# Kernel optimization log

Measured on AMD Instinct MI355X. Metric: run time of the kernel, lower is better.

Reference implementation:

```python
import jax, jax.numpy as jnp
import numpy as np

H = 64   # gru_hidden_dim == gnn_hidden_dim
F = 64   # node_feat_dim
K = 8    # k_nn
OUT = 32 # output_factor_dim
BN_EPS = 1e-5


def _gru_scan(x, Wih, Whh, bih, bhh):
    # x: [S, F] single sequence (torch bug makes GRU scan the b*n axis); returns [S, H]
    xp = x @ Wih.T + bih  # [S, 3H], gate order r,z,n (torch convention)
    def step(h, xt):
        hp = h @ Whh.T + bhh
        r = jax.nn.sigmoid(xt[:H] + hp[:H])
        z = jax.nn.sigmoid(xt[H:2 * H] + hp[H:2 * H])
        ng = jnp.tanh(xt[2 * H:] + r * hp[2 * H:])
        hn = (1.0 - z) * ng + z * h
        return hn, hn
    _, out = jax.lax.scan(step, jnp.zeros((H,), x.dtype), xp)
    return out


def _gcn_layer(x, row, col, w, W, b, n):
    # PyG GCNConv: out[col] += d^{-1/2}[row] * w * d^{-1/2}[col] * (x @ W.T)[row] + b
    xw = x @ W.T
    deg = jnp.zeros((n,), x.dtype).at[col].add(w)
    dinv = deg ** -0.5
    dinv = jnp.where(jnp.isinf(dinv), 0.0, dinv)
    norm = dinv[row] * w * dinv[col]
    out = jnp.zeros_like(xw).at[col].add(norm[:, None] * xw[row])
    return out + b


def setup_inputs() -> dict:
    key = jax.random.key(0)
    ks = jax.random.split(key, 20)
    s = 0.08  # ~ torch uniform(-1/sqrt(64), 1/sqrt(64)) scale
    d = {
        'x_seq': jax.random.normal(ks[0], (4, 8, F, 2048), jnp.float32),
        # gru_sim params
        'Wih_s': jax.random.normal(ks[1], (3 * H, F), jnp.float32) * s,
        'Whh_s': jax.random.normal(ks[2], (3 * H, H), jnp.float32) * s,
        'bih_s': jax.random.normal(ks[3], (3 * H,), jnp.float32) * s,
        'bhh_s': jax.random.normal(ks[4], (3 * H,), jnp.float32) * s,
        # gru params
        'Wih': jax.random.normal(ks[5], (3 * H, F), jnp.float32) * s,
        'Whh': jax.random.normal(ks[6], (3 * H, H), jnp.float32) * s,
        'bih': jax.random.normal(ks[7], (3 * H,), jnp.float32) * s,
        'bhh': jax.random.normal(ks[8], (3 * H,), jnp.float32) * s,
        # gcn1 / gcn2 params (GCNConv weight [out,in], bias [out])
        'W1': jax.random.normal(ks[9], (H, H), jnp.float32) * s,
        'b1': jnp.zeros((H,), jnp.float32),
        'W2': jax.random.normal(ks[10], (H, H), jnp.float32) * s,
        'b2': jnp.zeros((H,), jnp.float32),
        # batchnorm affine
        'gamma': jnp.ones((H,), jnp.float32),
        'beta': jnp.zeros((H,), jnp.float32),
        # predictor
        'Wp': jax.random.normal(ks[11], (OUT, H), jnp.float32) * s,
        'bp': jnp.zeros((OUT,), jnp.float32),
    }
    return d


def reference(x_seq, Wih_s, Whh_s, bih_s, bhh_s, Wih, Whh, bih, bhh,
              W1, b1, W2, b2, gamma, beta, Wp, bp):
    b, l, f, n = x_seq.shape
    # torch GRU is batch_first=True but fed [l, b*n, f]: it scans the b*n axis
    # as time and gru_out[-1] keeps only batch item l-1 -> only last time slice used.
    seq = x_seq[:, -1].transpose(0, 2, 1).reshape(b * n, f)  # [b*n, f]
    h = _gru_scan(seq, Wih_s, Whh_s, bih_s, bhh_s).reshape(b, n, H)      # gru_sim
    h_out = _gru_scan(seq, Wih, Whh, bih, bhh).reshape(b, n, H)          # gru

    # dynamic kNN graph from similarity
    sim = jnp.einsum('bni,bmi->bnm', h, h)
    eye = jnp.eye(n, dtype=bool)
    sim = jnp.where(eye[None], jnp.asarray(-1e9, sim.dtype), sim)
    vals, idx = jax.lax.top_k(sim, K)  # [b, n, K], sorted desc like torch.topk

    # edges: n*K knn edges + n unit-weight self loops (outer add_self_loops;
    # GCNConv's add_remaining_self_loops then adds nothing)
    row = jnp.concatenate([jnp.repeat(jnp.arange(n), K), jnp.arange(n)])

    def per_graph(v, ix, x):
        col = jnp.concatenate([ix.reshape(-1), jnp.arange(n)])
        w = jnp.concatenate([v.reshape(-1), jnp.ones((n,), v.dtype)])
        o1 = jax.nn.relu(_gcn_layer(x, row, col, w, W1, b1, n))
        o2 = jax.nn.relu(_gcn_layer(o1, row, col, w, W2, b2, n))
        return o2

    out2 = jax.vmap(per_graph)(vals, idx, h_out)  # [b, n, H]

    # BatchNorm1d (training mode: biased batch stats over b*n rows)
    flat = out2.reshape(b * n, H)
    mu = flat.mean(0)
    var = flat.var(0)
    normed = (flat - mu) / jnp.sqrt(var + BN_EPS) * gamma + beta

    out = normed @ Wp.T + bp
    return out.reshape(b, n, OUT)
```

## Files before the change

kernel.cpp:

```cpp
#include <hip/hip_runtime.h>
#include <hip/hip_bf16.h>

typedef __hip_bfloat16 bf16;

#define NB   4
#define NN   2048
#define NROW 8192
#define HD   64
#define G3   192
#define KNN  8
#define OUTD 32
#define SCHUNK 32
#define SBURN  96
#define NCH    256
#define SCH4   32
#define SBRN4  40
#define NCH4   256
#define TI   4
#define TOPB 256
#define XPR  32
#define SCR  32
#define TKR  16

#define OFF_FLAG  0u
#define OFF_DEG   64u
#define OFF_DINV  8256u
#define OFF_BNS   16448u
#define OFF_BNSQ  16512u
#define OFF_SCALE 16576u
#define OFF_SHIFT 16640u
#define OFF_VALS  16704u
#define OFF_IDX   82240u
#define OFF_A     147776u
#define OFF_C     672064u
#define OFF_XP0   1196352u
#define OFF_XP1   2769216u
#define OFF_END   4342080u

typedef __attribute__((ext_vector_type(8))) short short8v;
typedef __attribute__((ext_vector_type(4))) float f32x4;

__device__ __forceinline__ float sigmoidf_(float x) { return 1.f / (1.f + __expf(-x)); }
__device__ __forceinline__ float tanhf_(float x) {
    float e = __expf(-2.f * fabsf(x));
    float t = (1.f - e) / (1.f + e);
    return copysignf(t, x);
}
__device__ __forceinline__ float ld(const void* p, size_t i, int isbf) {
    return isbf ? __bfloat162float(((const bf16*)p)[i]) : ((const float*)p)[i];
}
__device__ __forceinline__ float bcast(float v, int k) {
    return __int_as_float(__builtin_amdgcn_readlane(__float_as_int(v), k));
}
__device__ __forceinline__ unsigned short bf16rne(float f) {
    unsigned u = __float_as_uint(f);
    return (unsigned short)((u + 0x7FFFu + ((u >> 16) & 1u)) >> 16);
}

__global__ void probe_kernel(const void* __restrict__ gamma, int* __restrict__ flag)
{
    unsigned w = ((const unsigned*)gamma)[0];
    *flag = (w == 0x3F800000u) ? 0 : 1;
}

__global__ __launch_bounds__(384) void xp_kernel(
    const void* __restrict__ x_seq,
    const void* __restrict__ Wih_s, const void* __restrict__ bih_s,
    const void* __restrict__ Wih,   const void* __restrict__ bih,
    float* __restrict__ xp0, float* __restrict__ xp1,
    const int* __restrict__ dtp)
{
    int isbf = *dtp;
    int row0 = blockIdx.x * XPR;
    int b = row0 >> 11, j0 = row0 & 2047;
    int t = threadIdx.x;

    __shared__ __align__(16) float S[XPR * 68];
    for (int idx = t; idx < XPR * HD; idx += 384) {
        int f = idx >> 5, jj = idx & (XPR - 1);
        S[jj * 68 + f] = ld(x_seq, (size_t)((b * 8 + 7) * 64 + f) * 2048 + (j0 + jj), isbf);
    }

    int g = t % G3;
    const void* W  = (t < G3) ? Wih_s : Wih;
    const void* bi = (t < G3) ? bih_s : bih;
    float* o = (t < G3) ? xp0 : xp1;
    float wreg[64];
    #pragma unroll
    for (int k = 0; k < 64; ++k) wreg[k] = ld(W, g * HD + k, isbf);
    float bias = ld(bi, g, isbf);
    __syncthreads();

    for (int jj = 0; jj < XPR; ++jj) {
        const float4* s4 = (const float4*)(S + jj * 68);
        float a0 = bias, a1 = 0.f, a2 = 0.f, a3 = 0.f;
        #pragma unroll
        for (int q = 0; q < 16; ++q) {
            float4 v = s4[q];
            a0 += wreg[4*q+0] * v.x;
            a1 += wreg[4*q+1] * v.y;
            a2 += wreg[4*q+2] * v.z;
            a3 += wreg[4*q+3] * v.w;
        }
        o[(size_t)(row0 + jj) * G3 + g] = (a0 + a1) + (a2 + a3);
    }
}

__global__ __launch_bounds__(128) void gru_scan_pack_kernel(
    const float* __restrict__ xp0, const float* __restrict__ xp1,
    const void* __restrict__ Whh_s, const void* __restrict__ bhh_s,
    const void* __restrict__ Whh,   const void* __restrict__ bhh,
    unsigned short* __restrict__ hAhi, unsigned short* __restrict__ hAlo,
    float* __restrict__ hC,
    const int* __restrict__ dtp)
{
    int isbf = *dtp;
    int gru = blockIdx.x >> 7;
    int pb  = blockIdx.x & 127;
    int w   = threadIdx.x >> 6;
    int L   = threadIdx.x & 63;
    int chunk = pb * 2 + w;
    const float* xpp = gru ? xp1 : xp0;
    const void* Wh   = gru ? Whh : Whh_s;
    const void* bh_p = gru ? bhh : bhh_s;

    __shared__ __align__(16) float4 SW4[64 * 64];

    for (int idx = threadIdx.x; idx < 64 * 64; idx += 128) {
        int k = idx >> 6, j = idx & 63;
        float4 v;
        v.x = ld(Wh, (size_t)j * 64 + k, isbf);
        v.y = ld(Wh, (size_t)(64 + j) * 64 + k, isbf);
        v.z = ld(Wh, (size_t)(128 + j) * 64 + k, isbf);
        v.w = 0.f;
        SW4[idx] = v;
    }
    float br  = ld(bh_p, L, isbf);
    float bz  = ld(bh_p, 64 + L, isbf);
    float bn_ = ld(bh_p, 128 + L, isbf);
    __syncthreads();

    int first = chunk * SCH4;
    int burn  = min(SBRN4, first);
    int start = first - burn;
    int steps = burn + SCH4;

    float hval = 0.f;
    size_t rb = (size_t)start * G3;
    float xr = xpp[rb + L];
    float xz = xpp[rb + 64 + L];
    float xn = xpp[rb + 128 + L];

    for (int t = 0; t < steps; ++t) {
        size_t nb = (size_t)min(start + t + 1, NROW - 1) * G3;
        float pxr = xpp[nb + L];
        float pxz = xpp[nb + 64 + L];
        float pxn = xpp[nb + 128 + L];

        float pr0 = br, pz0 = bz, pn0 = bn_;
        float pr1 = 0.f, pz1 = 0.f, pn1 = 0.f;
        #pragma unroll
        for (int k = 0; k < 64; k += 2) {
            float4 w0 = SW4[k * 64 + L];
            float4 w1 = SW4[(k + 1) * 64 + L];
            float b0 = bcast(hval, k);
            float b1 = bcast(hval, k + 1);
            pr0 += w0.x * b0; pz0 += w0.y * b0; pn0 += w0.z * b0;
            pr1 += w1.x * b1; pz1 += w1.y * b1; pn1 += w1.z * b1;
        }

        float r  = sigmoidf_(xr + pr0 + pr1);
        float z  = sigmoidf_(xz + pz0 + pz1);
        float ng = tanhf_(xn + r * (pn0 + pn1));
        hval = (1.f - z) * ng + z * hval;

        if (t >= burn) {
            size_t o = (size_t)(start + t) * HD + L;
            if (gru) {
                hC[o] = hval;
            } else {
                unsigned short hb = bf16rne(hval);
                float hf = __uint_as_float(((unsigned)hb) << 16);
                hAhi[o] = hb;
                hAlo[o] = bf16rne(hval - hf);
            }
        }
        xr = pxr; xz = pxz; xn = pxn;
    }
}

__global__ __launch_bounds__(192, 2) void gru_scan_fused_kernel(
    const void* __restrict__ x_seq,
    const void* __restrict__ Wih_s, const void* __restrict__ bih_s,
    const void* __restrict__ Whh_s, const void* __restrict__ bhh_s,
    const void* __restrict__ Wih,   const void* __restrict__ bih,
    const void* __restrict__ Whh,   const void* __restrict__ bhh,
    float* __restrict__ hA, float* __restrict__ hC,
    const int* __restrict__ dtp)
{
    int isbf = *dtp;
    int gru   = blockIdx.x >> 8;
    int chunk = blockIdx.x & 255;
    const void* Wh = gru ? Whh : Whh_s;
    const void* bh_p = gru ? bhh : bhh_s;
    const void* Wi = gru ? Wih : Wih_s;
    const void* bi_p = gru ? bih : bih_s;
    float* hout = gru ? hC : hA;

    int lane = threadIdx.x & 63;
    int w    = threadIdx.x >> 6;
    int g    = w * 64 + lane;

    float whh[64], wih[64];
    #pragma unroll
    for (int k = 0; k < 64; ++k) {
        whh[k] = ld(Wh, g * 64 + k, isbf);
        wih[k] = ld(Wi, g * 64 + k, isbf);
    }
    float bh = ld(bh_p, g, isbf);
    float bi = ld(bi_p, g, isbf);

    __shared__ float hs[64];
    __shared__ float ss[64];
    __shared__ float gr[64], gz[64], ga[64], gx[64];

    int first = chunk * SCHUNK;
    int burn  = min(SBURN, first);
    int start = first - burn;
    int steps = burn + SCHUNK;

    #define XIDX(r) ((size_t)((((r) >> 11) * 8 + 7) * 64 + lane) * 2048 + ((r) & 2047))
    float sf = 0.f;
    if (w == 0) {
        ss[lane] = ld(x_seq, XIDX(start), isbf);
        if (steps > 1) sf = ld(x_seq, XIDX(start + 1), isbf);
    }
    __syncthreads();

    float hval = 0.f;
    float sval = ss[lane];

    for (int t = 0; t < steps; ++t) {
        float a = bh, x = bi;
        #pragma unroll
        for (int k = 0; k < 64; ++k) {
            a += whh[k] * bcast(hval, k);
            x += wih[k] * bcast(sval, k);
        }
        if (w == 0)      gr[lane] = sigmoidf_(x + a);
        else if (w == 1) gz[lane] = sigmoidf_(x + a);
        else           { ga[lane] = a; gx[lane] = x; }
        __syncthreads();
        if (w == 0) {
            if (t + 1 < steps) {
                ss[lane] = sf;
                if (t + 2 < steps) sf = ld(x_seq, XIDX(start + t + 2), isbf);
            }
        } else if (w == 2) {
            float hn = (1.f - gz[lane]) * tanhf_(gx[lane] + gr[lane] * ga[lane])
                     + gz[lane] * hval;
            hs[lane] = hn;
            hval = hn;
            if (t >= burn) hout[(size_t)(start + t) * HD + lane] = hn;
        }
        __syncthreads();
        if (w != 2) hval = hs[lane];
        sval = ss[lane];
    }
    #undef XIDX
}

__device__ __forceinline__ void merge8(float tv[KNN], int tj[KNN], int off)
{
    float ov[KNN]; int oj[KNN];
    #pragma unroll
    for (int m = 0; m < KNN; ++m) {
        ov[m] = __shfl_xor(tv[m], off);
        oj[m] = __shfl_xor(tj[m], off);
    }
    #pragma unroll
    for (int m = 0; m < KNN; ++m) {
        if (ov[KNN - 1 - m] > tv[m]) { tv[m] = ov[KNN - 1 - m]; tj[m] = oj[KNN - 1 - m]; }
    }
    #pragma unroll
    for (int d = 4; d > 0; d >>= 1) {
        #pragma unroll
        for (int m = 0; m < KNN; ++m) {
            if ((m & d) == 0 && (m | d) < KNN) {
                int p = m | d;
                if (tv[p] > tv[m]) {
                    float fv = tv[m]; tv[m] = tv[p]; tv[p] = fv;
                    int fj = tj[m]; tj[m] = tj[p]; tj[p] = fj;
                }
            }
        }
    }
}

__global__ __launch_bounds__(512) void topk_mfma_kernel(
    const unsigned short* __restrict__ Ahi, const unsigned short* __restrict__ Alo,
    float* __restrict__ vals, int* __restrict__ idxs, float* __restrict__ deg)
{
    int bid = blockIdx.x;
    int row0 = bid * TKR;
    int bbase = row0 & ~(NN - 1);
    int rloc = row0 & (NN - 1);
    int t = threadIdx.x;
    int w = t >> 6, L = t & 63;
    int cL = L & 15, q = L >> 4;
    int chunk = q * 8;

    __shared__ float mv[8][TKR][KNN];
    __shared__ int   mj[8][TKR][KNN];

    size_t arow = (size_t)(row0 + cL) * HD;
    short8v ahi0 = *(const short8v*)(Ahi + arow + chunk);
    short8v ahi1 = *(const short8v*)(Ahi + arow + 32 + chunk);
    short8v alo0 = *(const short8v*)(Alo + arow + chunk);
    short8v alo1 = *(const short8v*)(Alo + arow + 32 + chunk);

    int jbase = w * 256;

    float tv[4][KNN]; int tj[4][KNN];
    #pragma unroll
    for (int e = 0; e < 4; ++e)
        #pragma unroll
        for (int m = 0; m < KNN; ++m) { tv[e][m] = -3e38f; tj[e][m] = 0; }

    #pragma unroll 1
    for (int strip = 0; strip < 4; ++strip) {
        #pragma unroll
        for (int g = 0; g < 4; ++g) {
            int j0 = jbase + strip * 64 + g * 16;
            size_t brow = (size_t)(bbase + j0 + cL) * HD;
            short8v bhi0 = *(const short8v*)(Ahi + brow + chunk);
            short8v bhi1 = *(const short8v*)(Ahi + brow + 32 + chunk);
            short8v blo0 = *(const short8v*)(Alo + brow + chunk);
            short8v blo1 = *(const short8v*)(Alo + brow + 32 + chunk);
            f32x4 accA = {0.f, 0.f, 0.f, 0.f};
            f32x4 accB = {0.f, 0.f, 0.f, 0.f};
            accA = __builtin_amdgcn_mfma_f32_16x16x32_bf16(ahi0, bhi0, accA, 0, 0, 0);
            accB = __builtin_amdgcn_mfma_f32_16x16x32_bf16(ahi0, blo0, accB, 0, 0, 0);
            accA = __builtin_amdgcn_mfma_f32_16x16x32_bf16(ahi1, bhi1, accA, 0, 0, 0);
            accB = __builtin_amdgcn_mfma_f32_16x16x32_bf16(ahi1, blo1, accB, 0, 0, 0);
            accA = __builtin_amdgcn_mfma_f32_16x16x32_bf16(alo0, bhi0, accA, 0, 0, 0);
            accB = __builtin_amdgcn_mfma_f32_16x16x32_bf16(alo1, bhi1, accB, 0, 0, 0);
            f32x4 acc = accA + accB;
            int jj = j0 + cL;
            #pragma unroll
            for (int e = 0; e < 4; ++e) {
                int r = q * 4 + e;
                float nv = (jj == rloc + r) ? -1e9f : acc[e];
                if (nv > tv[e][KNN - 1]) {
                    tv[e][KNN - 1] = nv; tj[e][KNN - 1] = jj;
                    #pragma unroll
                    for (int m = KNN - 1; m > 0; --m) {
                        if (tv[e][m] > tv[e][m - 1]) {
                            float fv = tv[e][m]; tv[e][m] = tv[e][m - 1]; tv[e][m - 1] = fv;
                            int fj = tj[e][m]; tj[e][m] = tj[e][m - 1]; tj[e][m - 1] = fj;
                        }
                    }
                }
            }
        }
    }

    #pragma unroll
    for (int e = 0; e < 4; ++e) {
        merge8(tv[e], tj[e], 1);
        merge8(tv[e], tj[e], 2);
        merge8(tv[e], tj[e], 4);
        merge8(tv[e], tj[e], 8);
    }
    if (cL == 0) {
        #pragma unroll
        for (int e = 0; e < 4; ++e)
            #pragma unroll
            for (int m = 0; m < KNN; ++m) {
                mv[w][q * 4 + e][m] = tv[e][m];
                mj[w][q * 4 + e][m] = tj[e][m];
            }
    }
    __syncthreads();

    if (w < 2) {
        int r = (w << 3) + (L >> 3);
        int p = L & 7;
        float fv[KNN]; int fj[KNN];
        #pragma unroll
        for (int m = 0; m < KNN; ++m) { fv[m] = mv[p][r][m]; fj[m] = mj[p][r][m]; }
        merge8(fv, fj, 1);
        merge8(fv, fj, 2);
        merge8(fv, fj, 4);
        if (p == 0) {
            int row = row0 + r;
            #pragma unroll
            for (int m = 0; m < KNN; ++m) {
                vals[(size_t)row * KNN + m] = fv[m];
                idxs[(size_t)row * KNN + m] = fj[m];
                atomicAdd(deg + bbase + fj[m], fv[m]);
            }
            atomicAdd(deg + row, 1.0f);
        }
    }
}

__global__ __launch_bounds__(TOPB, 2) void topk_kernel(
    const float* __restrict__ h,
    float* __restrict__ vals, int* __restrict__ idxs, float* __restrict__ deg)
{
    int bid = blockIdx.x;
    int b    = bid >> 9;
    int row0 = b * NN + (bid & 511) * TI;
    int i0 = row0 & 2047;
    int t = threadIdx.x;

    __shared__ __align__(16) float sim[TI][NN];
    __shared__ __align__(16) float hi[TI * HD];

    for (int q = t; q < TI * HD; q += TOPB)
        hi[q] = h[(size_t)(row0 + (q >> 6)) * HD + (q & 63)];
    __syncthreads();

    const float* hb = h + (size_t)b * NN * HD;
    const float4* hi4 = (const float4*)hi;
    #pragma unroll 1
    for (int j = t; j < NN; j += TOPB) {
        const float4* hr = (const float4*)(hb + (size_t)j * HD);
        float acc[TI];
        #pragma unroll
        for (int m = 0; m < TI; ++m) acc[m] = 0.f;
        #pragma unroll 4
        for (int q = 0; q < 16; ++q) {
            float4 v = hr[q];
            #pragma unroll
            for (int m = 0; m < TI; ++m) {
                float4 c = hi4[m * 16 + q];
                acc[m] += v.x*c.x + v.y*c.y + v.z*c.z + v.w*c.w;
            }
        }
        #pragma unroll
        for (int m = 0; m < TI; ++m)
            sim[m][j] = (j == i0 + m) ? -1e9f : acc[m];
    }
    __syncthreads();

    int w    = t >> 6;
    int lane = t & 63;
    int row  = row0 + w;

    float tv[KNN]; int tj[KNN];
    #pragma unroll
    for (int m = 0; m < KNN; ++m) { tv[m] = -3e38f; tj[m] = 0; }

    for (int k = 0; k < 32; ++k) {
        int j = lane + (k << 6);
        float nv = sim[w][j];
        if (nv > tv[KNN - 1]) {
            tv[KNN - 1] = nv; tj[KNN - 1] = j;
            #pragma unroll
            for (int m = KNN - 1; m > 0; --m) {
                if (tv[m] > tv[m - 1]) {
                    float fv = tv[m]; tv[m] = tv[m - 1]; tv[m - 1] = fv;
                    int fj = tj[m]; tj[m] = tj[m - 1]; tj[m - 1] = fj;
                }
            }
        }
    }

    #pragma unroll
    for (int off = 1; off < 64; off <<= 1) {
        float ov[KNN]; int oj[KNN];
        #pragma unroll
        for (int m = 0; m < KNN; ++m) {
            ov[m] = __shfl_xor(tv[m], off);
            oj[m] = __shfl_xor(tj[m], off);
        }
        #pragma unroll
        for (int m = 0; m < KNN; ++m) {
            if (ov[KNN - 1 - m] > tv[m]) { tv[m] = ov[KNN - 1 - m]; tj[m] = oj[KNN - 1 - m]; }
        }
        if (off < 32) {
            #pragma unroll
            for (int d = 4; d > 0; d >>= 1) {
                #pragma unroll
                for (int m = 0; m < KNN; ++m) {
                    if ((m & d) == 0 && (m | d) < KNN) {
                        int p = m | d;
                        if (tv[p] > tv[m]) {
                            float fv = tv[m]; tv[m] = tv[p]; tv[p] = fv;
                            int fj = tj[m]; tj[m] = tj[p]; tj[p] = fj;
                        }
                    }
                }
            }
        }
    }

    if (lane == 0) {
        #pragma unroll
        for (int m = 0; m < KNN; ++m) {
            vals[(size_t)row * KNN + m] = tv[m];
            idxs[(size_t)row * KNN + m] = tj[m];
            atomicAdd(deg + (b << 11) + tj[m], tv[m]);
        }
        atomicAdd(deg + row, 1.0f);
    }
}

__global__ void dinv_kernel(const float* __restrict__ deg, float* __restrict__ dinv)
{
    int g = blockIdx.x * 256 + threadIdx.x;
    if (g >= NROW) return;
    float d = deg[g];
    float r = 1.f / sqrtf(d);
    dinv[g] = isinf(r) ? 0.f : r;
}

__global__ __launch_bounds__(256) void scatter_kernel(
    const float* __restrict__ in, const void* __restrict__ W,
    const void* __restrict__ bias, int dorelu,
    const float* __restrict__ dinv,
    const float* __restrict__ vals, const int* __restrict__ idxs,
    float* __restrict__ acc, const int* __restrict__ dtp)
{
    int isbf = *dtp;
    int lane = threadIdx.x & 63;
    int w    = threadIdx.x >> 6;

    float wreg[64];
    #pragma unroll
    for (int k = 0; k < 64; ++k) wreg[k] = ld(W, lane * HD + k, isbf);
    float bb = ld(bias, lane, isbf);

    int row0 = blockIdx.x * SCR + w * (SCR / 4);
    #pragma unroll 1
    for (int rr = 0; rr < SCR / 4; ++rr) {
        int row = row0 + rr;
        int b = row >> 11;
        float x = in[(size_t)row * HD + lane];
        if (dorelu) x = fmaxf(x + bb, 0.f);
        float v0 = 0.f, v1 = 0.f, v2 = 0.f, v3 = 0.f;
        #pragma unroll
        for (int k = 0; k < 64; k += 4) {
            v0 += wreg[k]     * bcast(x, k);
            v1 += wreg[k + 1] * bcast(x, k + 1);
            v2 += wreg[k + 2] * bcast(x, k + 2);
            v3 += wreg[k + 3] * bcast(x, k + 3);
        }
        float v = (v0 + v1) + (v2 + v3);
        float di = dinv[row];
        atomicAdd(acc + (size_t)row * HD + lane, di * di * v);
        #pragma unroll
        for (int k = 0; k < KNN; ++k) {
            int c = idxs[(size_t)row * KNN + k];
            float wv = vals[(size_t)row * KNN + k];
            float nw = di * wv * dinv[(b << 11) + c];
            atomicAdd(acc + (size_t)((b << 11) + c) * HD + lane, nw * v);
        }
    }
}

__global__ __launch_bounds__(256) void bn_stats_kernel(
    const float* __restrict__ acc2, const void* __restrict__ bias,
    float* __restrict__ bns, float* __restrict__ bnsq,
    const int* __restrict__ dtp)
{
    int isbf = *dtp;
    int c  = threadIdx.x & 63;
    int wv = threadIdx.x >> 6;
    int row0 = blockIdx.x * 64 + wv * 16;
    float bb = ld(bias, c, isbf);
    float s = 0.f, s2 = 0.f;
    #pragma unroll
    for (int rr = 0; rr < 16; ++rr) {
        float v = fmaxf(acc2[(size_t)(row0 + rr) * HD + c] + bb, 0.f);
        s += v; s2 += v * v;
    }
    __shared__ float sv[4][64], sv2[4][64];
    sv[wv][c] = s; sv2[wv][c] = s2;
    __syncthreads();
    if (wv == 0) {
        s  = sv[0][c] + sv[1][c] + sv[2][c] + sv[3][c];
        s2 = sv2[0][c] + sv2[1][c] + sv2[2][c] + sv2[3][c];
        atomicAdd(bns + c, s);
        atomicAdd(bnsq + c, s2);
    }
}

__global__ void bn_final_kernel(const float* __restrict__ bns, const float* __restrict__ bnsq,
                                const void* __restrict__ gamma, const void* __restrict__ beta,
                                float* __restrict__ scale, float* __restrict__ shift,
                                const int* __restrict__ dtp)
{
    int isbf = *dtp;
    int c = threadIdx.x;
    float mu = bns[c] / (float)NROW;
    float var = fmaxf(bnsq[c] / (float)NROW - mu * mu, 0.f);
    float sc = ld(gamma, c, isbf) / sqrtf(var + 1e-5f);
    scale[c] = sc;
    shift[c] = ld(beta, c, isbf) - mu * sc;
}

__global__ void out_kernel(const float* __restrict__ acc2, const void* __restrict__ bias2,
                           const float* __restrict__ scale, const float* __restrict__ shift,
                           const void* __restrict__ Wp, const void* __restrict__ bp,
                           float* __restrict__ out, const int* __restrict__ dtp)
{
    int isbf = *dtp;
    int row0 = blockIdx.x * 2;
    int t = threadIdx.x;
    __shared__ float nl[2 * HD];
    for (int q = t; q < 2 * HD; q += 64) {
        int r = q >> 6, c = q & (HD - 1);
        float v = fmaxf(acc2[(size_t)(row0 + r) * HD + c] + ld(bias2, c, isbf), 0.f);
        nl[q] = v * scale[c] + shift[c];
    }
    __syncthreads();
    int rr = t >> 5, o = t & 31;
    float acc = ld(bp, o, isbf);
    #pragma unroll
    for (int k = 0; k < HD; ++k) acc += nl[rr * HD + k] * ld(Wp, o * HD + k, isbf);
    out[(size_t)(row0 + rr) * OUTD + o] = acc;
}

extern "C" void kernel_launch(void* const* d_in, const int* in_sizes, int n_in,
                              void* d_out, int out_size, void* d_ws, size_t ws_size,
                              hipStream_t stream)
{
    (void)in_sizes; (void)n_in; (void)out_size;
    const void* x_seq = d_in[0];
    const void* Wih_s = d_in[1];
    const void* Whh_s = d_in[2];
    const void* bih_s = d_in[3];
    const void* bhh_s = d_in[4];
    const void* Wih   = d_in[5];
    const void* Whh   = d_in[6];
    const void* bih   = d_in[7];
    const void* bhh   = d_in[8];
    const void* W1    = d_in[9];
    const void* b1    = d_in[10];
    const void* W2    = d_in[11];
    const void* b2    = d_in[12];
    const void* gamma = d_in[13];
    const void* beta  = d_in[14];
    const void* Wp    = d_in[15];
    const void* bp    = d_in[16];
    float* out = (float*)d_out;

    float* ws = (float*)d_ws;
    int*   dtp  = (int*)(ws + OFF_FLAG);
    float* deg  = ws + OFF_DEG;
    float* dinv = ws + OFF_DINV;
    float* bns  = ws + OFF_BNS;
    float* bnsq = ws + OFF_BNSQ;
    float* scale = ws + OFF_SCALE;
    float* shift = ws + OFF_SHIFT;
    float* vals = ws + OFF_VALS;
    int*   idxs = (int*)(ws + OFF_IDX);
    float* A    = ws + OFF_A;
    float* C    = ws + OFF_C;
    float* xp0  = ws + OFF_XP0;
    float* xp1  = ws + OFF_XP1;

    bool big_ws = ws_size >= (size_t)OFF_END * sizeof(float);

    probe_kernel<<<1, 1, 0, stream>>>(gamma, dtp);
    hipMemsetAsync(deg, 0, NROW * sizeof(float), stream);
    hipMemsetAsync(bns, 0, 2 * HD * sizeof(float), stream);

    if (big_ws) {
        xp_kernel<<<NROW / XPR, 384, 0, stream>>>(x_seq, Wih_s, bih_s, Wih, bih, xp0, xp1, dtp);
        gru_scan_pack_kernel<<<2 * (NCH4 / 2), 128, 0, stream>>>(
            xp0, xp1, Whh_s, bhh_s, Whh, bhh,
            (unsigned short*)A, (unsigned short*)A + (size_t)NROW * HD, C, dtp);
        topk_mfma_kernel<<<NROW / TKR, 512, 0, stream>>>(
            (unsigned short*)A, (unsigned short*)A + (size_t)NROW * HD, vals, idxs, deg);
    } else {
        gru_scan_fused_kernel<<<2 * NCH, 192, 0, stream>>>(x_seq, Wih_s, bih_s, Whh_s, bhh_s,
                                                           Wih, bih, Whh, bhh, A, C, dtp);
        topk_kernel<<<NROW / TI, TOPB, 0, stream>>>(A, vals, idxs, deg);
    }
    dinv_kernel<<<NROW / 256, 256, 0, stream>>>(deg, dinv);

    hipMemsetAsync(A, 0, (size_t)NROW * HD * sizeof(float), stream);
    scatter_kernel<<<NROW / SCR, 256, 0, stream>>>(C, W1, b1, 0, dinv, vals, idxs, A, dtp);

    hipMemsetAsync(C, 0, (size_t)NROW * HD * sizeof(float), stream);
    scatter_kernel<<<NROW / SCR, 256, 0, stream>>>(A, W2, b1, 1, dinv, vals, idxs, C, dtp);

    bn_stats_kernel<<<NROW / 64, 256, 0, stream>>>(C, b2, bns, bnsq, dtp);
    bn_final_kernel<<<1, HD, 0, stream>>>(bns, bnsq, gamma, beta, scale, shift, dtp);
    out_kernel<<<NROW / 2, 64, 0, stream>>>(C, b2, scale, shift, Wp, bp, out, dtp);
}
```

Before: 342.5 us.

## Transpose MFMA operands so each lane keeps one row's top-k list

Swaps the A/B operands of the MFMA so each lane's 4 accumulator values belong to one query row across 4 candidate columns, rather than 4 rows for one column. Each lane then keeps a single sorted top-8 list instead of four. Each group of 4 candidates is sorted with a small compare-exchange network, merged into the list with a bitonic-style half merge plus cleanup, and the cross-lane merge shrinks from four shuffle stages over four lists to two stages over one list. This cuts register pressure and divergent insertion work, but adds a fixed merge cost on every tile.

```diff
diff --git a/kernel.cpp b/kernel.cpp
--- a/kernel.cpp
+++ b/kernel.cpp
@@ -297,6 +297,26 @@
     }
 }
 
+__device__ __forceinline__ void cleanup8(float tv[KNN], int tj[KNN])
+{
+    #pragma unroll
+    for (int d = 4; d > 0; d >>= 1) {
+        #pragma unroll
+        for (int m = 0; m < KNN; ++m) {
+            if ((m & d) == 0 && (m | d) < KNN) {
+                int p = m | d;
+                if (tv[p] > tv[m]) {
+                    float fv = tv[m]; tv[m] = tv[p]; tv[p] = fv;
+                    int fj = tj[m]; tj[m] = tj[p]; tj[p] = fj;
+                }
+            }
+        }
+    }
+}
+
+#define CE4(a, b, ai, bi) \
+    if (b > a) { float tf_ = a; a = b; b = tf_; int ti_ = ai; ai = bi; bi = ti_; }
+
 __global__ __launch_bounds__(512) void topk_mfma_kernel(
     const unsigned short* __restrict__ Ahi, const unsigned short* __restrict__ Alo,
     float* __restrict__ vals, int* __restrict__ idxs, float* __restrict__ deg)
@@ -320,12 +340,11 @@
     short8v alo1 = *(const short8v*)(Alo + arow + 32 + chunk);
 
     int jbase = w * 256;
-
-    float tv[4][KNN]; int tj[4][KNN];
-    #pragma unroll
-    for (int e = 0; e < 4; ++e)
-        #pragma unroll
-        for (int m = 0; m < KNN; ++m) { tv[e][m] = -3e38f; tj[e][m] = 0; }
+    int myrow = rloc + cL;
+
+    float tv[KNN]; int tj[KNN];
+    #pragma unroll
+    for (int m = 0; m < KNN; ++m) { tv[m] = -3e38f; tj[m] = 0; }
 
     #pragma unroll 1
     for (int strip = 0; strip < 4; ++strip) {
@@ -339,47 +358,39 @@
             short8v blo1 = *(const short8v*)(Alo + brow + 32 + chunk);
             f32x4 accA = {0.f, 0.f, 0.f, 0.f};
             f32x4 accB = {0.f, 0.f, 0.f, 0.f};
-            accA = __builtin_amdgcn_mfma_f32_16x16x32_bf16(ahi0, bhi0, accA, 0, 0, 0);
-            accB = __builtin_amdgcn_mfma_f32_16x16x32_bf16(ahi0, blo0, accB, 0, 0, 0);
-            accA = __builtin_amdgcn_mfma_f32_16x16x32_bf16(ahi1, bhi1, accA, 0, 0, 0);
-            accB = __builtin_amdgcn_mfma_f32_16x16x32_bf16(ahi1, blo1, accB, 0, 0, 0);
-            accA = __builtin_amdgcn_mfma_f32_16x16x32_bf16(alo0, bhi0, accA, 0, 0, 0);
-            accB = __builtin_amdgcn_mfma_f32_16x16x32_bf16(alo1, bhi1, accB, 0, 0, 0);
+            accA = __builtin_amdgcn_mfma_f32_16x16x32_bf16(bhi0, ahi0, accA, 0, 0, 0);
+            accB = __builtin_amdgcn_mfma_f32_16x16x32_bf16(blo0, ahi0, accB, 0, 0, 0);
+            accA = __builtin_amdgcn_mfma_f32_16x16x32_bf16(bhi1, ahi1, accA, 0, 0, 0);
+            accB = __builtin_amdgcn_mfma_f32_16x16x32_bf16(blo1, ahi1, accB, 0, 0, 0);
+            accA = __builtin_amdgcn_mfma_f32_16x16x32_bf16(bhi0, alo0, accA, 0, 0, 0);
+            accB = __builtin_amdgcn_mfma_f32_16x16x32_bf16(bhi1, alo1, accB, 0, 0, 0);
             f32x4 acc = accA + accB;
-            int jj = j0 + cL;
-            #pragma unroll
-            for (int e = 0; e < 4; ++e) {
-                int r = q * 4 + e;
-                float nv = (jj == rloc + r) ? -1e9f : acc[e];
-                if (nv > tv[e][KNN - 1]) {
-                    tv[e][KNN - 1] = nv; tj[e][KNN - 1] = jj;
-                    #pragma unroll
-                    for (int m = KNN - 1; m > 0; --m) {
-                        if (tv[e][m] > tv[e][m - 1]) {
-                            float fv = tv[e][m]; tv[e][m] = tv[e][m - 1]; tv[e][m - 1] = fv;
-                            int fj = tj[e][m]; tj[e][m] = tj[e][m - 1]; tj[e][m - 1] = fj;
-                        }
-                    }
-                }
-            }
-        }
-    }
-
-    #pragma unroll
-    for (int e = 0; e < 4; ++e) {
-        merge8(tv[e], tj[e], 1);
-        merge8(tv[e], tj[e], 2);
-        merge8(tv[e], tj[e], 4);
-        merge8(tv[e], tj[e], 8);
-    }
-    if (cL == 0) {
-        #pragma unroll
-        for (int e = 0; e < 4; ++e)
-            #pragma unroll
-            for (int m = 0; m < KNN; ++m) {
-                mv[w][q * 4 + e][m] = tv[e][m];
-                mj[w][q * 4 + e][m] = tj[e][m];
-            }
+            int jq = j0 + (q << 2);
+            float cv0 = (jq + 0 == myrow) ? -1e9f : acc[0]; int cj0 = jq + 0;
+            float cv1 = (jq + 1 == myrow) ? -1e9f : acc[1]; int cj1 = jq + 1;
+            float cv2 = (jq + 2 == myrow) ? -1e9f : acc[2]; int cj2 = jq + 2;
+            float cv3 = (jq + 3 == myrow) ? -1e9f : acc[3]; int cj3 = jq + 3;
+            CE4(cv0, cv1, cj0, cj1)
+            CE4(cv2, cv3, cj2, cj3)
+            CE4(cv0, cv2, cj0, cj2)
+            CE4(cv1, cv3, cj1, cj3)
+            CE4(cv1, cv2, cj1, cj2)
+            if (cv3 > tv[4]) { tv[4] = cv3; tj[4] = cj3; }
+            if (cv2 > tv[5]) { tv[5] = cv2; tj[5] = cj2; }
+            if (cv1 > tv[6]) { tv[6] = cv1; tj[6] = cj1; }
+            if (cv0 > tv[7]) { tv[7] = cv0; tj[7] = cj0; }
+            cleanup8(tv, tj);
+        }
+    }
+
+    merge8(tv, tj, 16);
+    merge8(tv, tj, 32);
+    if (q == 0) {
+        #pragma unroll
+        for (int m = 0; m < KNN; ++m) {
+            mv[w][cL][m] = tv[m];
+            mj[w][cL][m] = tj[m];
+        }
     }
     __syncthreads();
 
```

Measured after the change: 333.3 us. -2.7%, faster.
